# Kernel tuning notes

Measured on AMD Instinct MI355X. Metric: run time of the kernel, lower is better.

## Reference

```python
import jax, jax.numpy as jnp
import numpy as np

B = 65536

def _conv(x, w, stride=(1, 1), padding='VALID', groups=1):
    return jax.lax.conv_general_dilated(
        x, w, window_strides=stride, padding=padding,
        dimension_numbers=('NCHW', 'OIHW', 'NCHW'), feature_group_count=groups)

def _lstm_step(x, h, c, w_ih, w_hh, b_ih, b_hh):
    # PyTorch gate order: i, f, g, o
    gates = x @ w_ih.T + h @ w_hh.T + b_ih + b_hh
    i, f, g, o = jnp.split(gates, 4, axis=-1)
    c_new = jax.nn.sigmoid(f) * c + jax.nn.sigmoid(i) * jnp.tanh(g)
    h_new = jax.nn.sigmoid(o) * jnp.tanh(c_new)
    return h_new, c_new


def setup_inputs() -> dict:
    key = jax.random.key(0)
    ks = jax.random.split(key, 32)
    s = 0.1
    inp = {
        'x': jax.random.normal(ks[0], (B, 3, 41), jnp.float32),
        'lstm1_h': jax.random.normal(ks[1], (B, 64), jnp.float32),
        'lstm1_b': jax.random.normal(ks[2], (B, 64), jnp.float32),
        'lstm2_h': jax.random.normal(ks[3], (B, 64), jnp.float32),
        'lstm2_b': jax.random.normal(ks[4], (B, 64), jnp.float32),
        # conv stack params
        'conv_dw_w': jax.random.normal(ks[5], (1, 1, 3, 3), jnp.float32) * s,
        'conv_pw_w': jax.random.normal(ks[6], (16, 1, 1, 1), jnp.float32) * s,
        'conv_pw_b': jax.random.normal(ks[7], (16,), jnp.float32) * s,
        'sep1_dw_w': jax.random.normal(ks[8], (16, 1, 1, 3), jnp.float32) * s,
        'sep1_pw_w': jax.random.normal(ks[9], (16, 16, 1, 1), jnp.float32) * s,
        'sep1_pw_b': jax.random.normal(ks[10], (16,), jnp.float32) * s,
        'sep2_dw_w': jax.random.normal(ks[11], (16, 1, 1, 3), jnp.float32) * s,
        'sep2_pw_w': jax.random.normal(ks[12], (16, 16, 1, 1), jnp.float32) * s,
        'sep2_pw_b': jax.random.normal(ks[13], (16,), jnp.float32) * s,
        # lstm1: input 80, hidden 64
        'w_ih1': jax.random.normal(ks[14], (256, 80), jnp.float32) * s,
        'w_hh1': jax.random.normal(ks[15], (256, 64), jnp.float32) * s,
        'b_ih1': jax.random.normal(ks[16], (256,), jnp.float32) * s,
        'b_hh1': jax.random.normal(ks[17], (256,), jnp.float32) * s,
        # lstm2: input 64, hidden 64
        'w_ih2': jax.random.normal(ks[18], (256, 64), jnp.float32) * s,
        'w_hh2': jax.random.normal(ks[19], (256, 64), jnp.float32) * s,
        'b_ih2': jax.random.normal(ks[20], (256,), jnp.float32) * s,
        'b_hh2': jax.random.normal(ks[21], (256,), jnp.float32) * s,
        # fc head
        'fc1_w': jax.random.normal(ks[22], (32, 128), jnp.float32) * s,
        'fc1_b': jax.random.normal(ks[23], (32,), jnp.float32) * s,
        'fc2_w': jax.random.normal(ks[24], (1, 32), jnp.float32) * s,
        'fc2_b': jax.random.normal(ks[25], (1,), jnp.float32) * s,
    }
    return inp


def reference(x, lstm1_h, lstm1_b, lstm2_h, lstm2_b,
              conv_dw_w, conv_pw_w, conv_pw_b,
              sep1_dw_w, sep1_pw_w, sep1_pw_b,
              sep2_dw_w, sep2_pw_w, sep2_pw_b,
              w_ih1, w_hh1, b_ih1, b_hh1,
              w_ih2, w_hh2, b_ih2, b_hh2,
              fc1_w, fc1_b, fc2_w, fc2_b):
    b = x.shape[0]
    y = x.reshape(b, 1, 3, 41)
    y = _conv(y, conv_dw_w)                                   # [B,1,1,39]
    y = _conv(y, conv_pw_w) + conv_pw_b[None, :, None, None]  # [B,16,1,39]
    y = jax.nn.relu(y)
    y = jax.lax.reduce_window(y, -jnp.inf, jax.lax.max,
                              (1, 1, 1, 3), (1, 1, 1, 2), 'VALID')  # [B,16,1,19]
    y = _conv(y, sep1_dw_w, stride=(2, 2), padding=((0, 0), (1, 1)), groups=16)  # [B,16,1,10]
    y = _conv(y, sep1_pw_w) + sep1_pw_b[None, :, None, None]
    y = jax.nn.relu(y)
    y = jnp.pad(y, ((0, 0), (0, 0), (0, 0), (0, 1)))          # [B,16,1,11]
    y = _conv(y, sep2_dw_w, stride=(2, 2), groups=16)         # [B,16,1,5]
    y = _conv(y, sep2_pw_w) + sep2_pw_b[None, :, None, None]
    y = jax.nn.relu(y)
    feat = y[:, :, 0, :].transpose(0, 2, 1).reshape(b, 80)    # permute(0,2,1) then flatten W*C
    h1, c1 = _lstm_step(feat, lstm1_h, lstm1_b, w_ih1, w_hh1, b_ih1, b_hh1)
    h2, c2 = _lstm_step(h1, lstm2_h, lstm2_b, w_ih2, w_hh2, b_ih2, b_hh2)
    z = jnp.concatenate([h2, h1], axis=-1)                    # [B,128]
    z = jax.nn.relu(z @ fc1_w.T + fc1_b)
    prob = jax.nn.sigmoid(z @ fc2_w.T + fc2_b)                # [B,1]
    return (prob[:, None, :], h1[None], c1[None], h2[None], c2[None])
```

## Files before the change

### kernel.cpp

```cpp
#include <hip/hip_runtime.h>

typedef unsigned short u16;
typedef __attribute__((ext_vector_type(8))) _Float16 f16x8;
typedef __attribute__((ext_vector_type(4))) float f32x4;

#define NT 256
#define BT 32
#define CBT 32
#define A1S 152
#define H1S 72
#define CFS 68

__device__ __forceinline__ u16 f2h(float f) {
  _Float16 h = (_Float16)f;
  union { _Float16 h; u16 u; } c; c.h = h; return c.u;
}
__device__ __forceinline__ float h2f(u16 v) {
  union { u16 u; _Float16 h; } c; c.u = v; return (float)c.h;
}
__device__ __forceinline__ float sigm(float x) { return 1.0f / (1.0f + __expf(-x)); }
__device__ __forceinline__ float tanh_(float x) {
  float ax = fabsf(x);
  float e = __expf(-2.0f * ax);
  float t = (1.0f - e) / (1.0f + e);
  return copysignf(t, x);
}
__device__ __forceinline__ uint2 packh4(float4 v) {
  return make_uint2((unsigned)f2h(v.x) | ((unsigned)f2h(v.y) << 16),
                    (unsigned)f2h(v.z) | ((unsigned)f2h(v.w) << 16));
}
__device__ __forceinline__ float4 unph4(uint2 p) {
  float4 r;
  r.x = h2f((u16)(p.x & 0xffff)); r.y = h2f((u16)(p.x >> 16));
  r.z = h2f((u16)(p.y & 0xffff)); r.w = h2f((u16)(p.y >> 16));
  return r;
}
__device__ __forceinline__ void bar() {
  asm volatile("s_waitcnt lgkmcnt(0)" ::: "memory");
  __builtin_amdgcn_s_barrier();
  asm volatile("" ::: "memory");
}

#define WS_W1   0
#define WS_W2   40960
#define WS_FC1  73728
#define WS_CW   77824
#define WS_BOFF 159744
#define WS_CF   161792
#define WS_FEAT_U16 81088


__global__ __launch_bounds__(NT) void prep(
    const float* __restrict__ wih1, const float* __restrict__ whh1,
    const float* __restrict__ wih2, const float* __restrict__ whh2,
    const float* __restrict__ fc1w,
    const float* __restrict__ bih1, const float* __restrict__ bhh1,
    const float* __restrict__ bih2, const float* __restrict__ bhh2,
    const float* __restrict__ dwWg, const float* __restrict__ pwWg, const float* __restrict__ pwBg,
    const float* __restrict__ s1dwg, const float* __restrict__ s1pwg, const float* __restrict__ s1pbg,
    const float* __restrict__ s2dwg, const float* __restrict__ s2pwg, const float* __restrict__ s2pbg,
    u16* __restrict__ wbf, float* __restrict__ bc, float* __restrict__ cf)
{
  int i = blockIdx.x * NT + threadIdx.x;
  if (i < 40960) {
    int j8 = i & 7, l = (i >> 3) & 63, rem = i >> 9;
    int kc = rem % 5, gw = rem / 5;
    int n = (gw >> 2) * 64 + (gw & 3) * 16 + (l & 15);
    int k = kc * 32 + (l >> 4) * 8 + j8;
    float v = 0.f;
    if (k < 80) v = wih1[n * 80 + k];
    else if (k < 144) v = whh1[n * 64 + (k - 80)];
    wbf[i] = f2h(v);
  } else if (i < 73728) {
    int t2 = i - 40960;
    int j8 = t2 & 7, l = (t2 >> 3) & 63, rem = t2 >> 9;
    int kc = rem & 3, gw = rem >> 2;
    int n = (gw >> 2) * 64 + (gw & 3) * 16 + (l & 15);
    int k = kc * 32 + (l >> 4) * 8 + j8;
    float v = (k < 64) ? wih2[n * 64 + k] : whh2[n * 64 + (k - 64)];
    wbf[i] = f2h(v);
  } else if (i < 77824) {
    int t2 = i - 73728;
    int j8 = t2 & 7, l = (t2 >> 3) & 63, rem = t2 >> 9;
    int kc = rem & 3, nt = rem >> 2;
    int n = nt * 16 + (l & 15);
    int k = kc * 32 + (l >> 4) * 8 + j8;
    int ks = (k < 64) ? k + 64 : k - 64;
    wbf[i] = f2h(fc1w[n * 128 + ks]);
  } else if (i < 79872) {
    int t2 = i - 77824;
    int frag = t2 >> 9, u = t2 & 511;
    int j8 = u & 7, l = (u >> 3) & 63;
    int co = l & 15, kk = (l >> 4) * 8 + j8;
    float v = 0.f;
    if (frag == 0) { int k = kk >> 4, ci = kk & 15; v = s1dwg[ci * 3 + k] * s1pwg[co * 16 + ci]; }
    else if (frag == 1) { if (kk < 16) v = s1dwg[kk * 3 + 2] * s1pwg[co * 16 + kk]; }
    else if (frag == 2) { int k = kk >> 4, ci = kk & 15; v = s2dwg[ci * 3 + k] * s2pwg[co * 16 + ci]; }
    else { if (kk < 16) v = s2dwg[kk * 3 + 2] * s2pwg[co * 16 + kk]; }
    wbf[i] = f2h(v);
  }
  if (i < 256)      bc[i] = bih1[i] + bhh1[i];
  else if (i < 512) bc[i] = bih2[i - 256] + bhh2[i - 256];
  if (i < 89) {
    float v;
    if (i < 16)      { float w = pwWg[i];      v = w > 0.f ? w : 0.f; }
    else if (i < 32) { float w = pwWg[i - 16]; v = w > 0.f ? 0.f : w; }
    else if (i < 48) v = pwBg[i - 32];
    else if (i < 64) v = s1pbg[i - 48];
    else if (i < 80) v = s2pbg[i - 64];
    else             v = dwWg[i - 80];
    cf[i] = v;
  }
}

#define CV_CW   0
#define CV_Y0   384
#define CV_XS   5504
#define CV_P    5504
#define CV_U1   5504
#define CV_FL   384
#define CV_SIZE 27008

__global__ __launch_bounds__(NT, 5) void convk(
    const float* __restrict__ xg, const u16* __restrict__ wbf,
    const float* __restrict__ cf, u16* __restrict__ featg)
{
  __shared__ __align__(16) unsigned char smem[CV_SIZE];
  const int t = threadIdx.x;
  const int blk = blockIdx.x;
  const int base = blk * CBT;

  float* cw = (float*)(smem + CV_CW);
  float* y0 = (float*)(smem + CV_Y0);
  float* xs = (float*)(smem + CV_XS);
  u16* pp  = (u16*)(smem + CV_P);
  u16* u1  = (u16*)(smem + CV_U1);
  u16* fl  = (u16*)(smem + CV_FL);

  const int lane = t & 63, wv = t >> 6, l15 = lane & 15, q16 = lane >> 4;

  const u16* Wf = wbf + WS_CW;
  f16x8 W1a = *(const f16x8*)(Wf + lane * 8);
  f16x8 W1b = *(const f16x8*)(Wf + 512 + lane * 8);
  f16x8 W2a = *(const f16x8*)(Wf + 1024 + lane * 8);
  f16x8 W2b = *(const f16x8*)(Wf + 1536 + lane * 8);

  if (t < 96) cw[t] = (t < 89) ? cf[t] : 0.f;
  {
    const float4* src = (const float4*)xg + (size_t)blk * 984;
    for (int i = t; i < 984; i += NT) *(float4*)(xs + i * 4) = src[i];
  }
  bar();

  {
    float d0 = cw[80], d1 = cw[81], d2 = cw[82], d3 = cw[83], d4 = cw[84],
          d5 = cw[85], d6 = cw[86], d7 = cw[87], d8 = cw[88];
    int b = t >> 3, w0 = (t & 7) * 5;
    const float* xb = xs + b * 123;
    float* yb = y0 + b * 40;
#pragma unroll
    for (int s = 0; s < 5; ++s) {
      int w = w0 + s;
      if (w < 39) {
        float v = d0 * xb[w]      + d1 * xb[w + 1]  + d2 * xb[w + 2]
                + d3 * xb[41 + w] + d4 * xb[42 + w] + d5 * xb[43 + w]
                + d6 * xb[82 + w] + d7 * xb[83 + w] + d8 * xb[84 + w];
        yb[w] = v;
      }
    }
  }
  bar();

  {
    uint4 z; z.x = z.y = z.z = z.w = 0u;
    if (t < 128) {
      int b = t >> 2, sub = t & 3;
      int col = (sub >> 1) ? 20 : 0;
      *(uint4*)(pp + (b * 21 + col) * 16 + (sub & 1) * 8) = z;
    }
    int b = t >> 3, u = t & 7, half = u >> 2, w5b = u & 3;
    float ph[8], pl[8], pb[8];
    ((float4*)ph)[0] = *(float4*)(cw + half * 8);
    ((float4*)ph)[1] = *(float4*)(cw + half * 8 + 4);
    ((float4*)pl)[0] = *(float4*)(cw + 16 + half * 8);
    ((float4*)pl)[1] = *(float4*)(cw + 16 + half * 8 + 4);
    ((float4*)pb)[0] = *(float4*)(cw + 32 + half * 8);
    ((float4*)pb)[1] = *(float4*)(cw + 32 + half * 8 + 4);
    const float* yb = y0 + b * 40;
#pragma unroll
    for (int s = 0; s < 5; ++s) {
      int w5 = w5b + s * 4;
      if (w5 < 19) {
        float a0 = yb[2 * w5], a1 = yb[2 * w5 + 1], a2 = yb[2 * w5 + 2];
        float mx = fmaxf(a0, fmaxf(a1, a2));
        float mn = fminf(a0, fminf(a1, a2));
        unsigned pk[4];
#pragma unroll
        for (int c = 0; c < 4; ++c) {
          float v0 = fmaxf(fmaf(ph[2 * c],     mx, fmaf(pl[2 * c],     mn, pb[2 * c])),     0.f);
          float v1 = fmaxf(fmaf(ph[2 * c + 1], mx, fmaf(pl[2 * c + 1], mn, pb[2 * c + 1])), 0.f);
          pk[c] = (unsigned)f2h(v0) | ((unsigned)f2h(v1) << 16);
        }
        uint4 st; st.x = pk[0]; st.y = pk[1]; st.z = pk[2]; st.w = pk[3];
        *(uint4*)(pp + (b * 21 + w5 + 1) * 16 + half * 8) = st;
      }
    }
  }
  bar();

  f32x4 acc5[5];
  {
    int kA = q16 >> 1, ciA = (q16 & 1) * 8;
#pragma unroll
    for (int s = 0; s < 5; ++s) {
      int tile = wv + s * 4;
      int rowA = tile * 16 + l15;
      int bA = rowA / 10, qA = rowA - bA * 10;
      f16x8 a0 = *(const f16x8*)(pp + (bA * 21 + 2 * qA + kA) * 16 + ciA);
      f16x8 a1 = *(const f16x8*)(pp + (bA * 21 + 2 * qA + 2) * 16 + ciA);
      f32x4 acc = {0.f, 0.f, 0.f, 0.f};
      acc = __builtin_amdgcn_mfma_f32_16x16x32_f16(a0, W1a, acc, 0, 0, 0);
      acc = __builtin_amdgcn_mfma_f32_16x16x32_f16(a1, W1b, acc, 0, 0, 0);
      acc5[s] = acc;
    }
  }
  bar();
  {
    if (t < 64) {
      uint4 z; z.x = z.y = z.z = z.w = 0u;
      *(uint4*)(u1 + ((t >> 1) * 11 + 10) * 16 + (t & 1) * 8) = z;
    }
    float sb1 = cw[48 + l15];
#pragma unroll
    for (int s = 0; s < 5; ++s) {
      int tile = wv + s * 4;
#pragma unroll
      for (int r = 0; r < 4; ++r) {
        int rowg = tile * 16 + q16 * 4 + r;
        int bC = rowg / 10, qC = rowg - bC * 10;
        u1[(bC * 11 + qC) * 16 + l15] = f2h(fmaxf(acc5[s][r] + sb1, 0.f));
      }
    }
  }
  bar();

  {
    float sb2 = cw[64 + l15];
    int kA = q16 >> 1, ciA = (q16 & 1) * 8;
    for (int tile = wv; tile < 10; tile += 4) {
      int rowA = tile * 16 + l15;
      int bA = rowA / 5, rA = rowA - bA * 5;
      f16x8 a0 = *(const f16x8*)(u1 + (bA * 11 + 2 * rA + kA) * 16 + ciA);
      f16x8 a1 = *(const f16x8*)(u1 + (bA * 11 + 2 * rA + 2) * 16 + ciA);
      f32x4 acc = {0.f, 0.f, 0.f, 0.f};
      acc = __builtin_amdgcn_mfma_f32_16x16x32_f16(a0, W2a, acc, 0, 0, 0);
      acc = __builtin_amdgcn_mfma_f32_16x16x32_f16(a1, W2b, acc, 0, 0, 0);
#pragma unroll
      for (int r = 0; r < 4; ++r) {
        int rowg = tile * 16 + q16 * 4 + r;
        int bC = rowg / 5, rC = rowg - bC * 5;
        fl[bC * 80 + rC * 16 + l15] = f2h(fmaxf(acc[r] + sb2, 0.f));
      }
    }
  }
  bar();

  {
    const uint4* s4 = (const uint4*)fl;
    uint4* d4 = (uint4*)(featg + (size_t)base * 80);
    for (int i = t; i < 320; i += NT) d4[i] = s4[i];
  }
}

#define LO_B1   0
#define LO_B2   256
#define LO_FC1B 512
#define LO_FC2W 544
#define LO_FC2B 576
#define LR_A1   2560
#define LR_H1N  12320
#define LR_C1F  16928
#define LR_C2F  21280
#define LSMEM   25632

__global__ __launch_bounds__(NT, 4) void lstmk(
    const float* __restrict__ h1g, const float* __restrict__ c1g,
    const float* __restrict__ h2g, const float* __restrict__ c2g,
    const float* __restrict__ fc1bg, const float* __restrict__ fc2wg, const float* __restrict__ fc2bg,
    const u16* __restrict__ wbf, const float* __restrict__ bc, const u16* __restrict__ featg,
    float* __restrict__ out, int B)
{
  __shared__ __align__(16) unsigned char smem[LSMEM];
  const int t = threadIdx.x;
  const int blk = blockIdx.x;
  const int base = blk * BT;

  float* sw = (float*)smem;
  u16* A1  = (u16*)(smem + LR_A1);
  u16* H1N = (u16*)(smem + LR_H1N);
  u16* c1f = (u16*)(smem + LR_C1F);
  u16* c2f = (u16*)(smem + LR_C2F);

  float* probO = out;
  float* h1o = out + B;
  float* c1o = out + B + B * 64;
  float* h2o = out + B + B * 128;
  float* c2o = out + B + B * 192;

  const u16* w1f = wbf + WS_W1;
  const u16* w2f = wbf + WS_W2;
  const u16* wFf = wbf + WS_FC1;

  const int w = t >> 6, lane = t & 63, q = lane >> 4, l15 = lane & 15;
  const int j = w * 16 + l15;

  {
    const float4* c1src = (const float4*)c1g + (size_t)blk * 512;
    const float4* c2src = (const float4*)c2g + (size_t)blk * 512;
#pragma unroll
    for (int k = 0; k < 2; ++k) {
      int i = t + k * 256, row = i >> 4, c4 = (i & 15) * 4;
      *(uint2*)(c1f + row * CFS + c4) = packh4(c1src[i]);
      *(uint2*)(c2f + row * CFS + c4) = packh4(c2src[i]);
    }
  }
  uint2 h2p[2];
  {
    const float4* hsrc = (const float4*)h2g + (size_t)blk * 512;
#pragma unroll
    for (int k = 0; k < 2; ++k) h2p[k] = packh4(hsrc[t + k * 256]);
  }
  for (int i = t; i < 512; i += NT) sw[i] = bc[i];
  for (int i = t; i < 32;  i += NT) sw[LO_FC1B + i] = fc1bg[i];
  for (int i = t; i < 32;  i += NT) sw[LO_FC2W + i] = fc2wg[i];
  if (t == 0) sw[LO_FC2B] = fc2bg[0];
  for (int i = t; i < 320; i += NT) {
    int m = i / 10, o = (i - m * 10) * 8;
    *(uint4*)(A1 + m * A1S + o) = *(const uint4*)(featg + (size_t)(base + m) * 80 + o);
  }
  {
    const float4* hsrc = (const float4*)h1g + (size_t)blk * 512;
#pragma unroll
    for (int k = 0; k < 2; ++k) {
      int i = t + k * 256, m = i >> 4, j4 = (i & 15) * 4;
      *(uint2*)(A1 + m * A1S + 80 + j4) = packh4(hsrc[i]);
    }
  }
  if (t < 32) {
    uint4 z; z.x = z.y = z.z = z.w = 0u;
    *(uint4*)(A1 + t * A1S + 144) = z;
  }
  if (t == 32) {
    uint4 z; z.x = z.y = z.z = z.w = 0u;
    *(uint4*)(A1 + 32 * A1S) = z;
  }
  bar();

  {
    f16x8 bf1[4][5];
#pragma unroll
    for (int g = 0; g < 4; ++g)
#pragma unroll
      for (int kc = 0; kc < 5; ++kc)
        bf1[g][kc] = *(const f16x8*)(w1f + (size_t)((((g * 4 + w) * 5 + kc) * 64) + lane) * 8);
    float bI = sw[LO_B1 + j], bF = sw[LO_B1 + 64 + j], bG = sw[LO_B1 + 128 + j], bO = sw[LO_B1 + 192 + j];

#pragma unroll 1
    for (int mt = 0; mt < 2; ++mt) {
      f32x4 acc[4];
#pragma unroll
      for (int g = 0; g < 4; ++g) { acc[g][0] = 0.f; acc[g][1] = 0.f; acc[g][2] = 0.f; acc[g][3] = 0.f; }
      const u16* aB = A1 + (mt * 16 + l15) * A1S + q * 8;
#pragma unroll
      for (int kc = 0; kc < 5; ++kc) {
        f16x8 af = *(const f16x8*)(aB + kc * 32);
#pragma unroll
        for (int g = 0; g < 4; ++g)
          acc[g] = __builtin_amdgcn_mfma_f32_16x16x32_f16(af, bf1[g][kc], acc[g], 0, 0, 0);
      }
#pragma unroll
      for (int r = 0; r < 4; ++r) {
        int m = mt * 16 + q * 4 + r;
        float iv = acc[0][r] + bI;
        float fv = acc[1][r] + bF;
        float gv = acc[2][r] + bG;
        float ov = acc[3][r] + bO;
        float cold = h2f(c1f[m * CFS + j]);
        float cn = sigm(fv) * cold + sigm(iv) * tanh_(gv);
        float hn = sigm(ov) * tanh_(cn);
        c1f[m * CFS + j] = f2h(cn);
        H1N[m * H1S + j] = f2h(hn);
      }
    }
  }
  bar();

  {
#pragma unroll
    for (int k = 0; k < 2; ++k) {
      int i = t + k * 256, m = i >> 4, j4 = (i & 15) * 4;
      *(uint2*)(A1 + m * A1S + 80 + j4) = h2p[k];
    }
  }
  bar();

  {
    f16x8 bf2[4][4];
#pragma unroll
    for (int g = 0; g < 4; ++g)
#pragma unroll
      for (int kc = 0; kc < 4; ++kc)
        bf2[g][kc] = *(const f16x8*)(w2f + (size_t)((((g * 4 + w) * 4 + kc) * 64) + lane) * 8);
    float bI = sw[LO_B2 + j], bF = sw[LO_B2 + 64 + j], bG = sw[LO_B2 + 128 + j], bO = sw[LO_B2 + 192 + j];

#pragma unroll 1
    for (int mt = 0; mt < 2; ++mt) {
      f32x4 acc[4];
#pragma unroll
      for (int g = 0; g < 4; ++g) { acc[g][0] = 0.f; acc[g][1] = 0.f; acc[g][2] = 0.f; acc[g][3] = 0.f; }
      const u16* aB1 = H1N + (mt * 16 + l15) * H1S + q * 8;
      const u16* aB2 = A1 + (mt * 16 + l15) * A1S + 80 + q * 8;
#pragma unroll
      for (int kc = 0; kc < 4; ++kc) {
        f16x8 af = (kc < 2) ? *(const f16x8*)(aB1 + kc * 32)
                            : *(const f16x8*)(aB2 + (kc - 2) * 32);
#pragma unroll
        for (int g = 0; g < 4; ++g)
          acc[g] = __builtin_amdgcn_mfma_f32_16x16x32_f16(af, bf2[g][kc], acc[g], 0, 0, 0);
      }
#pragma unroll
      for (int r = 0; r < 4; ++r) {
        int m = mt * 16 + q * 4 + r;
        float iv = acc[0][r] + bI;
        float fv = acc[1][r] + bF;
        float gv = acc[2][r] + bG;
        float ov = acc[3][r] + bO;
        float cold = h2f(c2f[m * CFS + j]);
        float cn = sigm(fv) * cold + sigm(iv) * tanh_(gv);
        float hn = sigm(ov) * tanh_(cn);
        c2f[m * CFS + j] = f2h(cn);
        A1[m * A1S + j] = f2h(hn);
      }
    }
  }
  bar();

  if (w < 2) {
    f32x4 accf[2];
#pragma unroll
    for (int nt = 0; nt < 2; ++nt) { accf[nt][0] = 0.f; accf[nt][1] = 0.f; accf[nt][2] = 0.f; accf[nt][3] = 0.f; }
    int m0 = w * 16;
#pragma unroll
    for (int kc = 0; kc < 4; ++kc) {
      f16x8 a = (kc < 2)
        ? *(const f16x8*)(H1N + (m0 + l15) * H1S + kc * 32 + q * 8)
        : *(const f16x8*)(A1 + (m0 + l15) * A1S + (kc - 2) * 32 + q * 8);
#pragma unroll
      for (int nt = 0; nt < 2; ++nt) {
        f16x8 bfr = *(const f16x8*)(wFf + (size_t)(((nt * 4 + kc) * 64) + lane) * 8);
        accf[nt] = __builtin_amdgcn_mfma_f32_16x16x32_f16(a, bfr, accf[nt], 0, 0, 0);
      }
    }
    float fw0 = sw[LO_FC2W + l15], fw1 = sw[LO_FC2W + 16 + l15];
    float fb0 = sw[LO_FC1B + l15], fb1 = sw[LO_FC1B + 16 + l15];
    float f2b = sw[LO_FC2B];
#pragma unroll
    for (int r = 0; r < 4; ++r) {
      float zv0 = fmaxf(accf[0][r] + fb0, 0.f);
      float zv1 = fmaxf(accf[1][r] + fb1, 0.f);
      float part = fmaf(zv0, fw0, zv1 * fw1);
      part += __shfl_xor(part, 1);
      part += __shfl_xor(part, 2);
      part += __shfl_xor(part, 4);
      part += __shfl_xor(part, 8);
      if (l15 == 0) probO[base + m0 + q * 4 + r] = sigm(part + f2b);
    }
  } else {
    int u = t - 128;
#pragma unroll
    for (int k = 0; k < 4; ++k) {
      int i = u + k * 128, row = i >> 4, c4 = (i & 15) * 4;
      size_t gb = (size_t)(base + row) * 64 + c4;
      *(float4*)(h1o + gb) = unph4(*(const uint2*)(H1N + row * H1S + c4));
      *(float4*)(c1o + gb) = unph4(*(const uint2*)(c1f + row * CFS + c4));
      *(float4*)(h2o + gb) = unph4(*(const uint2*)(A1 + row * A1S + c4));
      *(float4*)(c2o + gb) = unph4(*(const uint2*)(c2f + row * CFS + c4));
    }
  }
}

extern "C" void kernel_launch(void* const* d_in, const int* in_sizes, int n_in,
                              void* d_out, int out_size, void* d_ws, size_t ws_size,
                              hipStream_t stream) {
  (void)n_in; (void)out_size; (void)ws_size;
  int B = in_sizes[0] / 123;
  u16* wbf = (u16*)d_ws;
  float* bcm = (float*)((char*)d_ws + WS_BOFF);
  float* cfm = (float*)((char*)d_ws + WS_CF);
  u16* featg = (u16*)d_ws + WS_FEAT_U16;

  hipLaunchKernelGGL(prep, dim3(312), dim3(NT), 0, stream,
      (const float*)d_in[14], (const float*)d_in[15],
      (const float*)d_in[18], (const float*)d_in[19],
      (const float*)d_in[22],
      (const float*)d_in[16], (const float*)d_in[17],
      (const float*)d_in[20], (const float*)d_in[21],
      (const float*)d_in[5], (const float*)d_in[6], (const float*)d_in[7],
      (const float*)d_in[8], (const float*)d_in[9], (const float*)d_in[10],
      (const float*)d_in[11], (const float*)d_in[12], (const float*)d_in[13],
      wbf, bcm, cfm);

  hipLaunchKernelGGL(convk, dim3(B / CBT), dim3(NT), 0, stream,
      (const float*)d_in[0], wbf, cfm, featg);

  hipLaunchKernelGGL(lstmk, dim3(B / BT), dim3(NT), 0, stream,
      (const float*)d_in[1], (const float*)d_in[2],
      (const float*)d_in[3], (const float*)d_in[4],
      (const float*)d_in[23], (const float*)d_in[24], (const float*)d_in[25],
      wbf, bcm, featg,
      (float*)d_out, B);
}
```

Measured before the change: 228.3 us.

## Process two row tiles per LSTM block with all state loads issued upfront

The LSTM kernel now handles two 32-row tiles per block and issues every global load of the h/c state for both tiles at kernel start, keeping the packed fp16 values in registers. The second tile's loads are therefore in flight while the first tile computes. The h2 state gets its own shared buffer, which removes one barrier and the overwrite of the A1 region between the two LSTM steps. In exchange the kernel uses more registers and shared memory, and the grid is halved, which can lower occupancy and parallelism.

Result: slower. 256.8 us (+12.5%).

```diff
diff --git a/kernel.cpp b/kernel.cpp
--- a/kernel.cpp
+++ b/kernel.cpp
@@ -48,7 +48,6 @@
 #define WS_BOFF 159744
 #define WS_CF   161792
 #define WS_FEAT_U16 81088
-
 
 __global__ __launch_bounds__(NT) void prep(
     const float* __restrict__ wih1, const float* __restrict__ whh1,
@@ -281,80 +280,45 @@
 #define LR_H1N  12320
 #define LR_C1F  16928
 #define LR_C2F  21280
-#define LSMEM   25632
-
-__global__ __launch_bounds__(NT, 4) void lstmk(
-    const float* __restrict__ h1g, const float* __restrict__ c1g,
-    const float* __restrict__ h2g, const float* __restrict__ c2g,
-    const float* __restrict__ fc1bg, const float* __restrict__ fc2wg, const float* __restrict__ fc2bg,
-    const u16* __restrict__ wbf, const float* __restrict__ bc, const u16* __restrict__ featg,
-    float* __restrict__ out, int B)
+#define LR_H2B  25632
+#define LSMEM   29984
+
+__device__ __forceinline__ void lstm_stage(
+    unsigned char* smem, const u16* __restrict__ featg, int base, int t,
+    const uint2* c1p, const uint2* c2p, const uint2* h1p, const uint2* h2p)
 {
-  __shared__ __align__(16) unsigned char smem[LSMEM];
-  const int t = threadIdx.x;
-  const int blk = blockIdx.x;
-  const int base = blk * BT;
-
+  u16* A1  = (u16*)(smem + LR_A1);
+  u16* c1f = (u16*)(smem + LR_C1F);
+  u16* c2f = (u16*)(smem + LR_C2F);
+  u16* h2b = (u16*)(smem + LR_H2B);
+#pragma unroll
+  for (int k = 0; k < 2; ++k) {
+    int i = t + k * 256, row = i >> 4, c4 = (i & 15) * 4;
+    *(uint2*)(c1f + row * CFS + c4) = c1p[k];
+    *(uint2*)(c2f + row * CFS + c4) = c2p[k];
+    *(uint2*)(h2b + row * CFS + c4) = h2p[k];
+    *(uint2*)(A1 + row * A1S + 80 + c4) = h1p[k];
+  }
+  for (int i = t; i < 320; i += NT) {
+    int m = i / 10, o = (i - m * 10) * 8;
+    *(uint4*)(A1 + m * A1S + o) = *(const uint4*)(featg + (size_t)(base + m) * 80 + o);
+  }
+}
+
+__device__ __forceinline__ void lstm_tile(
+    unsigned char* smem, const u16* __restrict__ w1f, const u16* __restrict__ w2f,
+    const u16* __restrict__ wFf, int base, int t,
+    float* __restrict__ probO, float* __restrict__ h1o, float* __restrict__ c1o,
+    float* __restrict__ h2o, float* __restrict__ c2o)
+{
   float* sw = (float*)smem;
   u16* A1  = (u16*)(smem + LR_A1);
   u16* H1N = (u16*)(smem + LR_H1N);
   u16* c1f = (u16*)(smem + LR_C1F);
   u16* c2f = (u16*)(smem + LR_C2F);
-
-  float* probO = out;
-  float* h1o = out + B;
-  float* c1o = out + B + B * 64;
-  float* h2o = out + B + B * 128;
-  float* c2o = out + B + B * 192;
-
-  const u16* w1f = wbf + WS_W1;
-  const u16* w2f = wbf + WS_W2;
-  const u16* wFf = wbf + WS_FC1;
-
+  u16* h2b = (u16*)(smem + LR_H2B);
   const int w = t >> 6, lane = t & 63, q = lane >> 4, l15 = lane & 15;
   const int j = w * 16 + l15;
-
-  {
-    const float4* c1src = (const float4*)c1g + (size_t)blk * 512;
-    const float4* c2src = (const float4*)c2g + (size_t)blk * 512;
-#pragma unroll
-    for (int k = 0; k < 2; ++k) {
-      int i = t + k * 256, row = i >> 4, c4 = (i & 15) * 4;
-      *(uint2*)(c1f + row * CFS + c4) = packh4(c1src[i]);
-      *(uint2*)(c2f + row * CFS + c4) = packh4(c2src[i]);
-    }
-  }
-  uint2 h2p[2];
-  {
-    const float4* hsrc = (const float4*)h2g + (size_t)blk * 512;
-#pragma unroll
-    for (int k = 0; k < 2; ++k) h2p[k] = packh4(hsrc[t + k * 256]);
-  }
-  for (int i = t; i < 512; i += NT) sw[i] = bc[i];
-  for (int i = t; i < 32;  i += NT) sw[LO_FC1B + i] = fc1bg[i];
-  for (int i = t; i < 32;  i += NT) sw[LO_FC2W + i] = fc2wg[i];
-  if (t == 0) sw[LO_FC2B] = fc2bg[0];
-  for (int i = t; i < 320; i += NT) {
-    int m = i / 10, o = (i - m * 10) * 8;
-    *(uint4*)(A1 + m * A1S + o) = *(const uint4*)(featg + (size_t)(base + m) * 80 + o);
-  }
-  {
-    const float4* hsrc = (const float4*)h1g + (size_t)blk * 512;
-#pragma unroll
-    for (int k = 0; k < 2; ++k) {
-      int i = t + k * 256, m = i >> 4, j4 = (i & 15) * 4;
-      *(uint2*)(A1 + m * A1S + 80 + j4) = packh4(hsrc[i]);
-    }
-  }
-  if (t < 32) {
-    uint4 z; z.x = z.y = z.z = z.w = 0u;
-    *(uint4*)(A1 + t * A1S + 144) = z;
-  }
-  if (t == 32) {
-    uint4 z; z.x = z.y = z.z = z.w = 0u;
-    *(uint4*)(A1 + 32 * A1S) = z;
-  }
-  bar();
 
   {
     f16x8 bf1[4][5];
@@ -396,15 +360,6 @@
   bar();
 
   {
-#pragma unroll
-    for (int k = 0; k < 2; ++k) {
-      int i = t + k * 256, m = i >> 4, j4 = (i & 15) * 4;
-      *(uint2*)(A1 + m * A1S + 80 + j4) = h2p[k];
-    }
-  }
-  bar();
-
-  {
     f16x8 bf2[4][4];
 #pragma unroll
     for (int g = 0; g < 4; ++g)
@@ -419,7 +374,7 @@
 #pragma unroll
       for (int g = 0; g < 4; ++g) { acc[g][0] = 0.f; acc[g][1] = 0.f; acc[g][2] = 0.f; acc[g][3] = 0.f; }
       const u16* aB1 = H1N + (mt * 16 + l15) * H1S + q * 8;
-      const u16* aB2 = A1 + (mt * 16 + l15) * A1S + 80 + q * 8;
+      const u16* aB2 = h2b + (mt * 16 + l15) * CFS + q * 8;
 #pragma unroll
       for (int kc = 0; kc < 4; ++kc) {
         f16x8 af = (kc < 2) ? *(const f16x8*)(aB1 + kc * 32)
@@ -489,6 +444,80 @@
   }
 }
 
+__global__ __launch_bounds__(NT, 4) void lstmk(
+    const float* __restrict__ h1g, const float* __restrict__ c1g,
+    const float* __restrict__ h2g, const float* __restrict__ c2g,
+    const float* __restrict__ fc1bg, const float* __restrict__ fc2wg, const float* __restrict__ fc2bg,
+    const u16* __restrict__ wbf, const float* __restrict__ bc, const u16* __restrict__ featg,
+    float* __restrict__ out, int B)
+{
+  __shared__ __align__(16) unsigned char smem[LSMEM];
+  const int t = threadIdx.x;
+  const int blk = blockIdx.x;
+  const int base0 = blk * 2 * BT;
+  const int base1 = base0 + BT;
+
+  float* sw = (float*)smem;
+  u16* A1 = (u16*)(smem + LR_A1);
+
+  float* probO = out;
+  float* h1o = out + B;
+  float* c1o = out + B + B * 64;
+  float* h2o = out + B + B * 128;
+  float* c2o = out + B + B * 192;
+
+  const u16* w1f = wbf + WS_W1;
+  const u16* w2f = wbf + WS_W2;
+  const u16* wFf = wbf + WS_FC1;
+
+  uint2 c1p0[2], c2p0[2], h1p0[2], h2p0[2];
+  uint2 c1p1[2], c2p1[2], h1p1[2], h2p1[2];
+  {
+    const float4* c1s = (const float4*)c1g + (size_t)blk * 1024;
+    const float4* c2s = (const float4*)c2g + (size_t)blk * 1024;
+    const float4* h1s = (const float4*)h1g + (size_t)blk * 1024;
+    const float4* h2s = (const float4*)h2g + (size_t)blk * 1024;
+    float4 a0 = c1s[t], a1 = c1s[t + 256];
+    float4 b0 = c2s[t], b1 = c2s[t + 256];
+    float4 d0 = h1s[t], d1 = h1s[t + 256];
+    float4 e0 = h2s[t], e1 = h2s[t + 256];
+    float4 a2 = c1s[t + 512], a3 = c1s[t + 768];
+    float4 b2 = c2s[t + 512], b3 = c2s[t + 768];
+    float4 d2 = h1s[t + 512], d3 = h1s[t + 768];
+    float4 e2 = h2s[t + 512], e3 = h2s[t + 768];
+    c1p0[0] = packh4(a0); c1p0[1] = packh4(a1);
+    c2p0[0] = packh4(b0); c2p0[1] = packh4(b1);
+    h1p0[0] = packh4(d0); h1p0[1] = packh4(d1);
+    h2p0[0] = packh4(e0); h2p0[1] = packh4(e1);
+    c1p1[0] = packh4(a2); c1p1[1] = packh4(a3);
+    c2p1[0] = packh4(b2); c2p1[1] = packh4(b3);
+    h1p1[0] = packh4(d2); h1p1[1] = packh4(d3);
+    h2p1[0] = packh4(e2); h2p1[1] = packh4(e3);
+  }
+
+  for (int i = t; i < 512; i += NT) sw[i] = bc[i];
+  for (int i = t; i < 32;  i += NT) sw[LO_FC1B + i] = fc1bg[i];
+  for (int i = t; i < 32;  i += NT) sw[LO_FC2W + i] = fc2wg[i];
+  if (t == 0) sw[LO_FC2B] = fc2bg[0];
+  if (t < 32) {
+    uint4 z; z.x = z.y = z.z = z.w = 0u;
+    *(uint4*)(A1 + t * A1S + 144) = z;
+  }
+  if (t == 32) {
+    uint4 z; z.x = z.y = z.z = z.w = 0u;
+    *(uint4*)(A1 + 32 * A1S) = z;
+  }
+
+  lstm_stage(smem, featg, base0, t, c1p0, c2p0, h1p0, h2p0);
+  bar();
+  lstm_tile(smem, w1f, w2f, wFf, base0, t, probO, h1o, c1o, h2o, c2o);
+  bar();
+
+  lstm_stage(smem, featg, base1, t, c1p1, c2p1, h1p1, h2p1);
+  bar();
+  lstm_tile(smem, w1f, w2f, wFf, base1, t, probO, h1o, c1o, h2o, c2o);
+}
+
 extern "C" void kernel_launch(void* const* d_in, const int* in_sizes, int n_in,
                               void* d_out, int out_size, void* d_ws, size_t ws_size,
                               hipStream_t stream) {
@@ -513,7 +542,7 @@
   hipLaunchKernelGGL(convk, dim3(B / CBT), dim3(NT), 0, stream,
       (const float*)d_in[0], wbf, cfm, featg);
 
-  hipLaunchKernelGGL(lstmk, dim3(B / BT), dim3(NT), 0, stream,
+  hipLaunchKernelGGL(lstmk, dim3(B / (2 * BT)), dim3(NT), 0, stream,
       (const float*)d_in[1], (const float*)d_in[2],
       (const float*)d_in[3], (const float*)d_in[4],
       (const float*)d_in[23], (const float*)d_in[24], (const float*)d_in[25],
```
